# Performance work log

Measured on AMD Instinct MI355X. Metric: run time of the kernel, lower is better.

Reference implementation:

```python
import jax, jax.numpy as jnp
import numpy as np

B, K, N = 8, 4, 131072
DENSITY = 0.3
NEG_PAD = -1000.0
NEG_IDLE = -1.0e8


def setup_inputs() -> dict:
    rng = np.random.default_rng(0)
    mask_s = rng.random((B, K, N)) < DENSITY  # bool, per-slot variable counts
    mask_a = rng.random((B, K, N)) < DENSITY
    ts = int(mask_s.sum())
    ta = int(mask_a.sum())
    key = jax.random.key(0)
    k1, k2, k3, k4 = jax.random.split(key, 4)
    return {
        "rgb": jax.random.normal(k1, (ts, 3), dtype=jnp.float32),
        "logits_surface": jax.random.normal(k2, (ts, 1), dtype=jnp.float32),
        "logits_air": jax.random.normal(k3, (ta, 1), dtype=jnp.float32),
        "idle_states": (jax.random.uniform(k4, (B, K)) < 0.25).astype(jnp.float32),
        "mask_eval_surface": jnp.asarray(mask_s),
        "mask_eval_air": jnp.asarray(mask_a),
    }


def _expand(mask, values):
    # mask: (B,K,N) bool; values: (total, C) packed in row-major (b,k,n) mask order.
    # Returns (B,K,N,C) where masked positions hold their packed value (others garbage,
    # to be overwritten by the caller's jnp.where). Equivalent to the torch B*K scatter loop.
    m = mask.reshape(-1)
    pos = jnp.cumsum(m.astype(jnp.int32)) - 1  # packed index for each masked slot
    pos = jnp.clip(pos, 0, values.shape[0] - 1)
    return jnp.take(values, pos, axis=0).reshape(mask.shape + (values.shape[-1],))


def reference(rgb, logits_surface, logits_air, idle_states,
              mask_eval_surface, mask_eval_air):
    alive = (1.0 - idle_states)[:, :, None, None]  # (B,K,1,1)
    idle = idle_states[:, :, None, None]
    ms = mask_eval_surface[..., None]  # (B,K,N,1)
    ma = mask_eval_air[..., None]

    rgb_out = jnp.where(ms, _expand(mask_eval_surface, rgb) * alive, 0.0)
    logits_surface_out = jnp.where(
        ms, _expand(mask_eval_surface, logits_surface) * alive + idle * NEG_IDLE, NEG_PAD)
    logits_air_out = jnp.where(
        ma, _expand(mask_eval_air, logits_air) * alive + idle * NEG_IDLE, NEG_PAD)
    return rgb_out, logits_surface_out, logits_air_out
```

## Files before the change

kernel.cpp:

```cpp
#include <hip/hip_runtime.h>
#include <stdint.h>

#define NPER      131072
#define NTOT      4194304LL
#define CHUNK     2048
#define NBLK      2048
#define NEG_PAD   (-1000.0f)
#define NEG_IDLE  (-100000000.0f)

typedef unsigned long long u64;

__global__ __launch_bounds__(256, 8) void count_kernel(
    const int* __restrict__ ms, const int* __restrict__ ma,
    unsigned short* __restrict__ cmp, u64* __restrict__ totals)
{
    const int t = threadIdx.x, lane = t & 63, wave = t >> 6;
    const unsigned bid = blockIdx.x;
    const long long base = (long long)bid * CHUNK;

    const int4* ms4 = (const int4*)(ms + base);
    const int4* ma4 = (const int4*)(ma + base);
    int4 s0 = ms4[2 * t], s1 = ms4[2 * t + 1];
    int4 a0 = ma4[2 * t], a1 = ma4[2 * t + 1];
    unsigned sbits = (unsigned)(s0.x != 0)        | ((unsigned)(s0.y != 0) << 1)
                   | ((unsigned)(s0.z != 0) << 2) | ((unsigned)(s0.w != 0) << 3)
                   | ((unsigned)(s1.x != 0) << 4) | ((unsigned)(s1.y != 0) << 5)
                   | ((unsigned)(s1.z != 0) << 6) | ((unsigned)(s1.w != 0) << 7);
    unsigned abits = (unsigned)(a0.x != 0)        | ((unsigned)(a0.y != 0) << 1)
                   | ((unsigned)(a0.z != 0) << 2) | ((unsigned)(a0.w != 0) << 3)
                   | ((unsigned)(a1.x != 0) << 4) | ((unsigned)(a1.y != 0) << 5)
                   | ((unsigned)(a1.z != 0) << 6) | ((unsigned)(a1.w != 0) << 7);

    cmp[bid * 256u + (unsigned)t] = (unsigned short)(sbits | (abits << 8));

    unsigned cnt = __popc(sbits) | (__popc(abits) << 16);
    #pragma unroll
    for (int o = 32; o; o >>= 1) cnt += __shfl_down(cnt, o, 64);
    __shared__ unsigned lds[4];
    if (lane == 0) lds[wave] = cnt;
    __syncthreads();
    if (t == 0) {
        unsigned tot = lds[0] + lds[1] + lds[2] + lds[3];
        totals[bid] = (u64)(tot & 0xffffu) | ((u64)(tot >> 16) << 32);
    }
}

__global__ __launch_bounds__(256, 8) void expand_kernel(
    const float* __restrict__ rgb, const float* __restrict__ lsurf,
    const float* __restrict__ lair, const float* __restrict__ idle,
    const unsigned short* __restrict__ cmp, const u64* __restrict__ totals,
    unsigned rgb_max, unsigned ts_max, unsigned ta_max,
    float* __restrict__ out_rgb, float* __restrict__ out_ls, float* __restrict__ out_la)
{
    __shared__ unsigned wsum[4];
    __shared__ u64 wacc[4];
    const int t = threadIdx.x, lane = t & 63, wave = t >> 6;
    const unsigned bid = blockIdx.x;
    const long long base = (long long)bid * CHUNK;

    unsigned pk = cmp[bid * 256u + (unsigned)t];
    u64 acc = 0;
    #pragma unroll
    for (int j = 0; j < 8; ++j) {
        unsigned idx = (unsigned)t * 8u + (unsigned)j;
        acc += (idx < bid) ? totals[idx] : 0ULL;
    }
    const int bk = (int)(base >> 17);
    const float idle_v = idle[bk];

    unsigned sbits = pk & 0xffu, abits = pk >> 8;
    unsigned cnt = __popc(sbits) | (__popc(abits) << 16);

    unsigned x = cnt;
    #pragma unroll
    for (int o = 1; o < 64; o <<= 1) {
        unsigned y = __shfl_up(x, o, 64);
        if (lane >= o) x += y;
    }
    if (lane == 63) wsum[wave] = x;

    #pragma unroll
    for (int o = 32; o; o >>= 1) acc += __shfl_down(acc, o, 64);
    if (lane == 0) wacc[wave] = acc;
    __syncthreads();
    unsigned w0 = wsum[0], w1 = wsum[1], w2 = wsum[2], w3 = wsum[3];
    unsigned pre   = (wave > 0 ? w0 : 0u) + (wave > 1 ? w1 : 0u) + (wave > 2 ? w2 : 0u);
    unsigned tExcl = pre + x - cnt;
    u64 basesum = wacc[0] + wacc[1] + wacc[2] + wacc[3];
    unsigned excS = (unsigned)(basesum & 0xffffffffULL);
    unsigned excA = (unsigned)(basesum >> 32);

    const float alive     = 1.0f - idle_v;
    const float idle_term = idle_v * NEG_IDLE;
    unsigned rs = excS + (tExcl & 0xffffu);
    unsigned ra = excA + (tExcl >> 16);
    const long long e0 = base + 8LL * t;

    float ls_b[8]  __attribute__((aligned(16)));
    float la_b[8]  __attribute__((aligned(16)));
    float rg_b[24] __attribute__((aligned(16)));
    #pragma unroll
    for (int j = 0; j < 8; ++j) {
        if ((sbits >> j) & 1u) {
            unsigned pr = rs < rgb_max ? rs : rgb_max;
            long long q = 3LL * pr;
            rg_b[3 * j]     = rgb[q]     * alive;
            rg_b[3 * j + 1] = rgb[q + 1] * alive;
            rg_b[3 * j + 2] = rgb[q + 2] * alive;
            unsigned pl = rs < ts_max ? rs : ts_max;
            ls_b[j] = lsurf[pl] * alive + idle_term;
            rs++;
        } else {
            rg_b[3 * j] = 0.f; rg_b[3 * j + 1] = 0.f; rg_b[3 * j + 2] = 0.f;
            ls_b[j] = NEG_PAD;
        }
        if ((abits >> j) & 1u) {
            unsigned pa = ra < ta_max ? ra : ta_max;
            la_b[j] = lair[pa] * alive + idle_term;
            ra++;
        } else {
            la_b[j] = NEG_PAD;
        }
    }

    float4* ols = (float4*)(out_ls + e0);
    ols[0] = ((float4*)ls_b)[0]; ols[1] = ((float4*)ls_b)[1];
    float4* ola = (float4*)(out_la + e0);
    ola[0] = ((float4*)la_b)[0]; ola[1] = ((float4*)la_b)[1];
    float4* org = (float4*)(out_rgb + 3 * e0);
    #pragma unroll
    for (int q = 0; q < 6; ++q) org[q] = ((float4*)rg_b)[q];
}

extern "C" void kernel_launch(void* const* d_in, const int* in_sizes, int n_in,
                              void* d_out, int out_size, void* d_ws, size_t ws_size,
                              hipStream_t stream)
{
    const float* rgb   = (const float*)d_in[0];
    const float* lsurf = (const float*)d_in[1];
    const float* lair  = (const float*)d_in[2];
    const float* idle  = (const float*)d_in[3];
    const int*   ms    = (const int*)d_in[4];
    const int*   ma    = (const int*)d_in[5];

    unsigned rgb_max = (unsigned)(in_sizes[0] / 3 - 1);
    unsigned ts_max  = (unsigned)(in_sizes[1] - 1);
    unsigned ta_max  = (unsigned)(in_sizes[2] - 1);

    float* out     = (float*)d_out;
    float* out_rgb = out;
    float* out_ls  = out + NTOT * 3;
    float* out_la  = out_ls + NTOT;

    u64* totals = (u64*)d_ws;
    unsigned short* cmp = (unsigned short*)((char*)d_ws + 16384);

    count_kernel<<<NBLK, 256, 0, stream>>>(ms, ma, cmp, totals);
    expand_kernel<<<NBLK, 256, 0, stream>>>(rgb, lsurf, lair, idle, cmp, totals,
                                            rgb_max, ts_max, ta_max,
                                            out_rgb, out_ls, out_la);
}
```

Baseline: 161.3 us.

## Remap expand kernel so consecutive threads handle consecutive elements, staging rgb in LDS

In the expand kernel, each thread no longer owns 8 contiguous elements. Threads now process elements strided by 256, so consecutive lanes gather consecutive packed inputs and write coalesced scalar stores to both logits outputs. Per-element packed offsets come from an LDS copy of the bitmasks and per-thread prefix sums plus a popcount. RGB results are staged in a 12KB LDS buffer and written out as float4 in two halves, which costs extra barriers and LDS use that may lower occupancy.

```diff
diff --git a/kernel.cpp b/kernel.cpp
--- a/kernel.cpp
+++ b/kernel.cpp
@@ -54,6 +54,10 @@
 {
     __shared__ unsigned wsum[4];
     __shared__ u64 wacc[4];
+    __shared__ unsigned packLDS[256];
+    __shared__ unsigned prefLDS[256];
+    __shared__ float    rgbLDS[3072];
+
     const int t = threadIdx.x, lane = t & 63, wave = t >> 6;
     const unsigned bid = blockIdx.x;
     const long long base = (long long)bid * CHUNK;
@@ -65,11 +69,10 @@
         unsigned idx = (unsigned)t * 8u + (unsigned)j;
         acc += (idx < bid) ? totals[idx] : 0ULL;
     }
-    const int bk = (int)(base >> 17);
-    const float idle_v = idle[bk];
+    const float idle_v = idle[(int)(base >> 17)];
 
-    unsigned sbits = pk & 0xffu, abits = pk >> 8;
-    unsigned cnt = __popc(sbits) | (__popc(abits) << 16);
+    packLDS[t] = pk;
+    unsigned cnt = __popc(pk & 0xffu) | (__popc(pk >> 8) << 16);
 
     unsigned x = cnt;
     #pragma unroll
@@ -78,58 +81,63 @@
         if (lane >= o) x += y;
     }
     if (lane == 63) wsum[wave] = x;
-
     #pragma unroll
     for (int o = 32; o; o >>= 1) acc += __shfl_down(acc, o, 64);
     if (lane == 0) wacc[wave] = acc;
     __syncthreads();
-    unsigned w0 = wsum[0], w1 = wsum[1], w2 = wsum[2], w3 = wsum[3];
-    unsigned pre   = (wave > 0 ? w0 : 0u) + (wave > 1 ? w1 : 0u) + (wave > 2 ? w2 : 0u);
-    unsigned tExcl = pre + x - cnt;
+    unsigned pre = (wave > 0 ? wsum[0] : 0u) + (wave > 1 ? wsum[1] : 0u)
+                 + (wave > 2 ? wsum[2] : 0u);
+    prefLDS[t] = pre + x - cnt;
     u64 basesum = wacc[0] + wacc[1] + wacc[2] + wacc[3];
-    unsigned excS = (unsigned)(basesum & 0xffffffffULL);
-    unsigned excA = (unsigned)(basesum >> 32);
+    const unsigned excS = (unsigned)(basesum & 0xffffffffULL);
+    const unsigned excA = (unsigned)(basesum >> 32);
+    __syncthreads();
 
     const float alive     = 1.0f - idle_v;
     const float idle_term = idle_v * NEG_IDLE;
-    unsigned rs = excS + (tExcl & 0xffffu);
-    unsigned ra = excA + (tExcl >> 16);
-    const long long e0 = base + 8LL * t;
+    const int  sub = t >> 3, b = t & 7;
+    const unsigned sm = (1u << b) - 1u;
 
-    float ls_b[8]  __attribute__((aligned(16)));
-    float la_b[8]  __attribute__((aligned(16)));
-    float rg_b[24] __attribute__((aligned(16)));
     #pragma unroll
-    for (int j = 0; j < 8; ++j) {
-        if ((sbits >> j) & 1u) {
-            unsigned pr = rs < rgb_max ? rs : rgb_max;
-            long long q = 3LL * pr;
-            rg_b[3 * j]     = rgb[q]     * alive;
-            rg_b[3 * j + 1] = rgb[q + 1] * alive;
-            rg_b[3 * j + 2] = rgb[q + 2] * alive;
-            unsigned pl = rs < ts_max ? rs : ts_max;
-            ls_b[j] = lsurf[pl] * alive + idle_term;
-            rs++;
-        } else {
-            rg_b[3 * j] = 0.f; rg_b[3 * j + 1] = 0.f; rg_b[3 * j + 2] = 0.f;
-            ls_b[j] = NEG_PAD;
+    for (int h = 0; h < 2; ++h) {
+        #pragma unroll
+        for (int r = 0; r < 4; ++r) {
+            const int e = (h * 4 + r) * 256 + t;
+            const int p = ((h * 4 + r) << 5) + sub;
+            unsigned w  = packLDS[p];
+            unsigned pv = prefLDS[p];
+            unsigned rs = excS + (pv & 0xffffu) + __popc(w & sm);
+            unsigned ra = excA + (pv >> 16)     + __popc((w >> 8) & sm);
+            unsigned s = (w >> b) & 1u, a = (w >> (8 + b)) & 1u;
+
+            float lso = NEG_PAD, lao = NEG_PAD;
+            const int li = r * 768 + 3 * t;
+            if (s) {
+                unsigned pr = rs < rgb_max ? rs : rgb_max;
+                long long q = 3LL * pr;
+                rgbLDS[li]     = rgb[q]     * alive;
+                rgbLDS[li + 1] = rgb[q + 1] * alive;
+                rgbLDS[li + 2] = rgb[q + 2] * alive;
+                unsigned pl = rs < ts_max ? rs : ts_max;
+                lso = lsurf[pl] * alive + idle_term;
+            } else {
+                rgbLDS[li] = 0.f; rgbLDS[li + 1] = 0.f; rgbLDS[li + 2] = 0.f;
+            }
+            if (a) {
+                unsigned pa = ra < ta_max ? ra : ta_max;
+                lao = lair[pa] * alive + idle_term;
+            }
+            out_ls[base + e] = lso;
+            out_la[base + e] = lao;
         }
-        if ((abits >> j) & 1u) {
-            unsigned pa = ra < ta_max ? ra : ta_max;
-            la_b[j] = lair[pa] * alive + idle_term;
-            ra++;
-        } else {
-            la_b[j] = NEG_PAD;
-        }
+        __syncthreads();
+        float4* dst = (float4*)(out_rgb + 3 * base) + (h ? 768 : 0);
+        const float4* src = (const float4*)rgbLDS;
+        dst[t]       = src[t];
+        dst[t + 256] = src[t + 256];
+        dst[t + 512] = src[t + 512];
+        __syncthreads();
     }
-
-    float4* ols = (float4*)(out_ls + e0);
-    ols[0] = ((float4*)ls_b)[0]; ols[1] = ((float4*)ls_b)[1];
-    float4* ola = (float4*)(out_la + e0);
-    ola[0] = ((float4*)la_b)[0]; ola[1] = ((float4*)la_b)[1];
-    float4* org = (float4*)(out_rgb + 3 * e0);
-    #pragma unroll
-    for (int q = 0; q < 6; ++q) org[q] = ((float4*)rg_b)[q];
 }
 
 extern "C" void kernel_launch(void* const* d_in, const int* in_sizes, int n_in,
```

Result: faster. 148.9 us (-7.7%).
